# Optimization experiments

Measured on AMD Instinct MI355X. Metric: run time of the kernel, lower is better.

Reference implementation:

```python
import jax, jax.numpy as jnp
import numpy as np

MAX_ITER = 10
EPS = 1e-4


def setup_inputs() -> dict:
    key = jax.random.key(0)
    k1, k2, k3 = jax.random.split(key, 3)
    B, N, M = 64, 1024, 1024
    s = jax.random.uniform(k1, (B, N, M), dtype=jnp.float32)
    nrows = jax.random.randint(k2, (B,), 0, N, dtype=jnp.int64 if jax.config.read('jax_enable_x64') else jnp.int32)
    ncols = jax.random.randint(k3, (B,), 0, M, dtype=nrows.dtype)
    return {"s": s, "nrows": nrows, "ncols": ncols}


def _sinkhorn(s, nrows, ncols):
    # Faithful to torch Sinkhorn.forward with exp=False, dummy_row=False.
    # The torch code builds [B,N,N]/[B,M,M] block-of-ones matrices and matmuls;
    # mathematically this is a masked column-sum (even iters) / row-sum (odd iters)
    # over the valid nrows[b] x ncols[b] block, followed by division inside the
    # block and zeroing outside it.
    B, N, M = s.shape
    row_mask = jnp.arange(N)[None, :] < nrows[:, None]            # [B, N]
    col_mask = jnp.arange(M)[None, :] < ncols[:, None]            # [B, M]
    mask = row_mask[:, :, None] & col_mask[:, None, :]            # [B, N, M]

    out = s + EPS
    for i in range(MAX_ITER):
        if i % 2 == 0:
            # column sums over valid rows -> [B, 1, M]
            sm = jnp.sum(jnp.where(row_mask[:, :, None], out, 0.0), axis=1, keepdims=True)
        else:
            # row sums over valid cols -> [B, N, 1]
            sm = jnp.sum(jnp.where(col_mask[:, None, :], out, 0.0), axis=2, keepdims=True)
        sm = jnp.where(sm == 0, 1.0, sm)  # guard (only affects masked-out entries)
        out = jnp.where(mask, out / sm, 0.0)
    return out


def reference(s, nrows, ncols):
    return _sinkhorn(s, nrows, ncols)
```

## Files before the change

### kernel.cpp

```cpp
#include <hip/hip_runtime.h>
#include <hip/hip_fp16.h>

#define EPS 1e-4f
constexpr int N_DIM  = 1024;
constexpr int M_DIM  = 1024;
constexpr int BATCH  = 64;
constexpr int NB     = 1024;
constexpr int NPHASE = 5;
constexpr int WPAD   = 256;
constexpr int CH     = 16;
constexpr int Q8MIN  = 64;


typedef float v4f __attribute__((ext_vector_type(4)));
__device__ __forceinline__ float4 ntload4(const float* p) {
    v4f v = __builtin_nontemporal_load((const v4f*)p);
    return make_float4(v[0], v[1], v[2], v[3]);
}
__device__ __forceinline__ void ntstore4(float* p, float4 q) {
    v4f v = {q.x, q.y, q.z, q.w};
    __builtin_nontemporal_store(v, (v4f*)p);
}

__device__ __forceinline__ unsigned enc8(float v) {
    int u = (int)__float_as_uint(v) + 0x00040000 - 0x3C000000;
    int b = u >> 19;
    return (unsigned)min(max(b, 16), 127);
}
__device__ __forceinline__ float dec8(unsigned b) {
    return b ? __uint_as_float((b << 19) + 0x3C000000u) : 0.f;
}

__global__ void zero_cnt(unsigned int* cnt) {
    const int t = threadIdx.x;
    if (t < NPHASE * BATCH) cnt[t] = 0u;
}

__device__ __forceinline__ void bat_barrier(unsigned int* cnt, int idx,
                                            unsigned int nact) {
    __syncthreads();
    if (threadIdx.x == 0) {
        __threadfence();
        atomicAdd(&cnt[idx], 1u);
        while (__hip_atomic_load(&cnt[idx], __ATOMIC_ACQUIRE,
                                 __HIP_MEMORY_SCOPE_AGENT) < nact)
            __builtin_amdgcn_s_sleep(8);
    }
    __syncthreads();
    __threadfence();
}

__device__ __forceinline__ void tp_store(__half* tp, size_t idx, float4 v) {
    union { __half2 h2[2]; uint2 u; } pk;
    pk.h2[0] = __floats2half2_rn(v.x, v.y);
    pk.h2[1] = __floats2half2_rn(v.z, v.w);
    *(uint2*)(tp + idx) = pk.u;
}

__global__ __launch_bounds__(256, 4)
void sinkhorn_prop(const float* __restrict__ s,
                   const int* __restrict__ nrows,
                   const int* __restrict__ ncols,
                   __half* __restrict__ h,
                   __half* __restrict__ tp0,
                   __half* __restrict__ tp1,
                   unsigned int* __restrict__ cnt,
                   float* __restrict__ out)
{
    const int tid = threadIdx.x, lane = tid & 63, wv = tid >> 6;
    __shared__ int sR[BATCH];
    __shared__ int sNb[BATCH];
    __shared__ int sPfx[BATCH + 1];

    if (tid < BATCH) sR[tid] = nrows[tid];
    __syncthreads();
    if (tid == 0) {
        long tot = 0;
        for (int i = 0; i < BATCH; ++i) tot += sR[i] + WPAD;
        int acc = 0;
        for (int i = 0; i < BATCH; ++i) {
            int nb = 1 + (int)(((long)(NB - BATCH) * (sR[i] + WPAD)) / tot);
            sNb[i] = nb; sPfx[i] = acc; acc += nb;
        }
        sPfx[BATCH] = acc;
    }
    __syncthreads();

    const int g = blockIdx.x;
    if (g >= sPfx[BATCH]) return;
    int b = BATCH - 1;
    for (int i = 0; i < BATCH; ++i) { if (g < sPfx[i + 1]) { b = i; break; } }
    const int l   = g - sPfx[b];
    const int nbb = sNb[b];
    const int R = sR[b], C = ncols[b];
    const size_t base = (size_t)b * N_DIM * M_DIM;
    const float4 z4 = make_float4(0.f, 0.f, 0.f, 0.f);

    for (int n = R + l; n < N_DIM; n += nbb)
        ntstore4(out + base + (size_t)n * M_DIM + tid * 4, z4);
    if (R == 0) return;

    const int CR = (R + nbb - 1) / nbb;
    const unsigned int nact = (unsigned int)((R + CR - 1) / CR);
    if ((unsigned int)l >= nact) return;
    const int n0 = l * CR;
    const int rows = min(R - n0, CR);
    const bool hi = (C > 512);
    const bool q8 = (R >= Q8MIN && C >= Q8MIN);
    const int g0 = sPfx[b];
    unsigned char* __restrict__ h8 = (unsigned char*)(h + base);

    __shared__ float clds[M_DIM];
    __shared__ float tp_lds[4][M_DIM];

    {
        const int m = tid * 4;
        float4 acc = z4;
        if (m < C) {
            for (int nn = 0; nn < rows; ++nn) {
                const size_t roff = (size_t)(n0 + nn) * M_DIM + m;
                float4 v = ntload4(s + base + roff);
                v.x += EPS;
                v.y = (m + 1 < C) ? v.y + EPS : 0.f;
                v.z = (m + 2 < C) ? v.z + EPS : 0.f;
                v.w = (m + 3 < C) ? v.w + EPS : 0.f;
                acc.x += v.x; acc.y += v.y; acc.z += v.z; acc.w += v.w;
                if (q8) {
                    unsigned b0 = enc8(v.x);
                    unsigned b1 = (v.y > 0.f) ? enc8(v.y) : 0u;
                    unsigned b2 = (v.z > 0.f) ? enc8(v.z) : 0u;
                    unsigned b3 = (v.w > 0.f) ? enc8(v.w) : 0u;
                    *(unsigned*)(h8 + roff) = b0 | (b1 << 8) | (b2 << 16) | (b3 << 24);
                } else {
                    union { __half2 h2[2]; uint2 u2; } pk;
                    pk.h2[0] = __floats2half2_rn(v.x, v.y);
                    pk.h2[1] = __floats2half2_rn(v.z, v.w);
                    *(uint2*)(h + base + roff) = pk.u2;
                }
            }
        } else if (m < 512 || hi) {
            for (int nn = 0; nn < rows; ++nn) {
                const size_t roff = (size_t)(n0 + nn) * M_DIM + m;
                if (q8) *(unsigned*)(h8 + roff) = 0u;
                else    *(uint2*)(h + base + roff) = make_uint2(0u, 0u);
            }
        }
        if (m < 512 || hi)
            tp_store(tp0, (size_t)g * M_DIM + m, acc);
    }
    bat_barrier(cnt, 0 * BATCH + b, nact);

    const __half* tpIn  = tp0;
    __half*       tpOut = tp1;
    float crlo[8], crhi[8];

    for (int step = 0; step < 4; ++step) {
        {
            const int m = tid * 4;
            if (m < 512 || hi) {
                float4 sum = z4;
                for (unsigned int cc = 0; cc < nact; ++cc) {
                    uint2 raw = *(const uint2*)(tpIn + (size_t)(g0 + cc) * M_DIM + m);
                    const __half2* hp = (const __half2*)&raw;
                    float2 f0 = __half22float2(hp[0]);
                    float2 f1 = __half22float2(hp[1]);
                    sum.x += f0.x; sum.y += f0.y; sum.z += f1.x; sum.w += f1.y;
                }
                float4 cv;
                cv.x = (sum.x == 0.f) ? 1.f : 1.f / sum.x;
                cv.y = (sum.y == 0.f) ? 1.f : 1.f / sum.y;
                cv.z = (sum.z == 0.f) ? 1.f : 1.f / sum.z;
                cv.w = (sum.w == 0.f) ? 1.f : 1.f / sum.w;
                *(float4*)&clds[m] = cv;
            }
        }
        __syncthreads();
        {
            float4 a  = *(const float4*)&clds[lane * 8];
            float4 bb = *(const float4*)&clds[lane * 8 + 4];
            crlo[0]=a.x; crlo[1]=a.y; crlo[2]=a.z; crlo[3]=a.w;
            crlo[4]=bb.x; crlo[5]=bb.y; crlo[6]=bb.z; crlo[7]=bb.w;
            if (hi) {
                float4 d = *(const float4*)&clds[512 + lane * 8];
                float4 e = *(const float4*)&clds[512 + lane * 8 + 4];
                crhi[0]=d.x; crhi[1]=d.y; crhi[2]=d.z; crhi[3]=d.w;
                crhi[4]=e.x; crhi[5]=e.y; crhi[6]=e.z; crhi[7]=e.w;
            }
        }

        float tplo[8] = {0,0,0,0,0,0,0,0};
        float tphi[8] = {0,0,0,0,0,0,0,0};

        for (int nn = wv; nn < rows; nn += 4) {
            float flo[8], fhi[8];
            if (q8) {
                const unsigned char* hrow = h8 + (size_t)(n0 + nn) * M_DIM;
                uint2 rlo = *(const uint2*)(hrow + lane * 8);
#pragma unroll
                for (int k = 0; k < 4; ++k) flo[k]     = dec8((rlo.x >> (8*k)) & 0xffu);
#pragma unroll
                for (int k = 0; k < 4; ++k) flo[4 + k] = dec8((rlo.y >> (8*k)) & 0xffu);
                if (hi) {
                    uint2 rhi = *(const uint2*)(hrow + 512 + lane * 8);
#pragma unroll
                    for (int k = 0; k < 4; ++k) fhi[k]     = dec8((rhi.x >> (8*k)) & 0xffu);
#pragma unroll
                    for (int k = 0; k < 4; ++k) fhi[4 + k] = dec8((rhi.y >> (8*k)) & 0xffu);
                }
            } else {
                const __half* hrow = h + base + (size_t)(n0 + nn) * M_DIM;
                uint4 rlo = *(const uint4*)(hrow + lane * 8);
                const __half2* hp = (const __half2*)&rlo;
#pragma unroll
                for (int k = 0; k < 4; ++k) {
                    float2 f = __half22float2(hp[k]);
                    flo[2*k] = f.x; flo[2*k+1] = f.y;
                }
                if (hi) {
                    uint4 rhi = *(const uint4*)(hrow + 512 + lane * 8);
                    const __half2* hq = (const __half2*)&rhi;
#pragma unroll
                    for (int k = 0; k < 4; ++k) {
                        float2 f = __half22float2(hq[k]);
                        fhi[2*k] = f.x; fhi[2*k+1] = f.y;
                    }
                }
            }
            float dot = 0.f;
#pragma unroll
            for (int k = 0; k < 8; ++k) dot += flo[k] * crlo[k];
            if (hi) {
#pragma unroll
                for (int k = 0; k < 8; ++k) dot += fhi[k] * crhi[k];
            }
#pragma unroll
            for (int off = 32; off; off >>= 1) dot += __shfl_xor(dot, off);
            const float r = (dot == 0.f) ? 1.f : 1.f / dot;
#pragma unroll
            for (int k = 0; k < 8; ++k) tplo[k] += flo[k] * r;
            if (hi) {
#pragma unroll
                for (int k = 0; k < 8; ++k) tphi[k] += fhi[k] * r;
            }
        }

#pragma unroll
        for (int k = 0; k < 8; ++k) tp_lds[wv][lane * 8 + k] = tplo[k];
        if (hi) {
#pragma unroll
            for (int k = 0; k < 8; ++k) tp_lds[wv][512 + lane * 8 + k] = tphi[k];
        }
        __syncthreads();
        {
            const int m = tid * 4;
            if (m < 512 || hi) {
                float4 s0 = *(const float4*)&tp_lds[0][m];
                float4 s1 = *(const float4*)&tp_lds[1][m];
                float4 s2 = *(const float4*)&tp_lds[2][m];
                float4 s3 = *(const float4*)&tp_lds[3][m];
                tp_store(tpOut, (size_t)g * M_DIM + m,
                         make_float4(s0.x+s1.x+s2.x+s3.x, s0.y+s1.y+s2.y+s3.y,
                                     s0.z+s1.z+s2.z+s3.z, s0.w+s1.w+s2.w+s3.w));
            }
        }
        bat_barrier(cnt, (1 + step) * BATCH + b, nact);
        const __half* ti = tpOut; tpOut = (__half*)tpIn; tpIn = ti;
    }

    {
        const int m = tid * 4;
        if (m < 512 || hi) {
            float4 sum = z4;
            for (unsigned int cc = 0; cc < nact; ++cc) {
                uint2 raw = *(const uint2*)(tpIn + (size_t)(g0 + cc) * M_DIM + m);
                const __half2* hp = (const __half2*)&raw;
                float2 f0 = __half22float2(hp[0]);
                float2 f1 = __half22float2(hp[1]);
                sum.x += f0.x; sum.y += f0.y; sum.z += f1.x; sum.w += f1.y;
            }
            float4 cv;
            cv.x = (sum.x == 0.f) ? 1.f : 1.f / sum.x;
            cv.y = (sum.y == 0.f) ? 1.f : 1.f / sum.y;
            cv.z = (sum.z == 0.f) ? 1.f : 1.f / sum.z;
            cv.w = (sum.w == 0.f) ? 1.f : 1.f / sum.w;
            *(float4*)&clds[m] = cv;
        }
    }
    __syncthreads();
    {
        float4 a  = *(const float4*)&clds[lane * 8];
        float4 bb = *(const float4*)&clds[lane * 8 + 4];
        crlo[0]=a.x; crlo[1]=a.y; crlo[2]=a.z; crlo[3]=a.w;
        crlo[4]=bb.x; crlo[5]=bb.y; crlo[6]=bb.z; crlo[7]=bb.w;
        if (hi) {
            float4 d = *(const float4*)&clds[512 + lane * 8];
            float4 e = *(const float4*)&clds[512 + lane * 8 + 4];
            crhi[0]=d.x; crhi[1]=d.y; crhi[2]=d.z; crhi[3]=d.w;
            crhi[4]=e.x; crhi[5]=e.y; crhi[6]=e.z; crhi[7]=e.w;
        }
    }
    for (int nn = wv; nn < rows; nn += 4) {
        const int n = n0 + nn;
        float* orow = out + base + (size_t)n * M_DIM;
        float flo[8], fhi[8];
        if (q8) {
            const unsigned char* hrow = h8 + (size_t)n * M_DIM;
            uint2 rlo = *(const uint2*)(hrow + lane * 8);
#pragma unroll
            for (int k = 0; k < 4; ++k) flo[k]     = dec8((rlo.x >> (8*k)) & 0xffu);
#pragma unroll
            for (int k = 0; k < 4; ++k) flo[4 + k] = dec8((rlo.y >> (8*k)) & 0xffu);
            if (hi) {
                uint2 rhi = *(const uint2*)(hrow + 512 + lane * 8);
#pragma unroll
                for (int k = 0; k < 4; ++k) fhi[k]     = dec8((rhi.x >> (8*k)) & 0xffu);
#pragma unroll
                for (int k = 0; k < 4; ++k) fhi[4 + k] = dec8((rhi.y >> (8*k)) & 0xffu);
            }
        } else {
            const __half* hrow = h + base + (size_t)n * M_DIM;
            uint4 rlo = *(const uint4*)(hrow + lane * 8);
            const __half2* hp = (const __half2*)&rlo;
#pragma unroll
            for (int k = 0; k < 4; ++k) {
                float2 f = __half22float2(hp[k]);
                flo[2*k] = f.x; flo[2*k+1] = f.y;
            }
            if (hi) {
                uint4 rhi = *(const uint4*)(hrow + 512 + lane * 8);
                const __half2* hq = (const __half2*)&rhi;
#pragma unroll
                for (int k = 0; k < 4; ++k) {
                    float2 f = __half22float2(hq[k]);
                    fhi[2*k] = f.x; fhi[2*k+1] = f.y;
                }
            }
        }
        float dot = 0.f;
#pragma unroll
        for (int k = 0; k < 8; ++k) dot += flo[k] * crlo[k];
        if (hi) {
#pragma unroll
            for (int k = 0; k < 8; ++k) dot += fhi[k] * crhi[k];
        }
#pragma unroll
        for (int off = 32; off; off >>= 1) dot += __shfl_xor(dot, off);
        const float r = (dot == 0.f) ? 1.f : 1.f / dot;

        ntstore4(orow + lane * 8,     make_float4(flo[0]*r*crlo[0], flo[1]*r*crlo[1],
                                                  flo[2]*r*crlo[2], flo[3]*r*crlo[3]));
        ntstore4(orow + lane * 8 + 4, make_float4(flo[4]*r*crlo[4], flo[5]*r*crlo[5],
                                                  flo[6]*r*crlo[6], flo[7]*r*crlo[7]));
        float4 o2 = z4, o3 = z4;
        if (hi) {
            o2 = make_float4(fhi[0]*r*crhi[0], fhi[1]*r*crhi[1],
                             fhi[2]*r*crhi[2], fhi[3]*r*crhi[3]);
            o3 = make_float4(fhi[4]*r*crhi[4], fhi[5]*r*crhi[5],
                             fhi[6]*r*crhi[6], fhi[7]*r*crhi[7]);
        }
        ntstore4(orow + 512 + lane * 8,     o2);
        ntstore4(orow + 512 + lane * 8 + 4, o3);
    }
}

constexpr int FCROWS = N_DIM / CH;

__global__ __launch_bounds__(256)
void conv_col0(const float* __restrict__ s, const int* __restrict__ nrows,
               const int* __restrict__ ncols, __half* __restrict__ h,
               float* __restrict__ tp0) {
    const int b  = blockIdx.y;
    const int mt = blockIdx.x & 3;
    const int ch = blockIdx.x >> 2;
    const int R = nrows[b], C = ncols[b];
    const int n0 = ch * FCROWS;
    if (n0 >= R) return;
    const int lane = threadIdx.x & 63, wv = threadIdx.x >> 6;
    const int m = mt * 256 + lane * 4;
    const int nend = min(R, n0 + FCROWS);
    const size_t base = (size_t)b * N_DIM * M_DIM;

    float4 acc = make_float4(0.f, 0.f, 0.f, 0.f);
    if (mt * 256 < C) {
        for (int n = n0 + wv; n < nend; n += 4) {
            float4 v = *(const float4*)(s + base + (size_t)n * M_DIM + m);
            v.x = (m + 0 < C) ? v.x + EPS : 0.f;
            v.y = (m + 1 < C) ? v.y + EPS : 0.f;
            v.z = (m + 2 < C) ? v.z + EPS : 0.f;
            v.w = (m + 3 < C) ? v.w + EPS : 0.f;
            acc.x += v.x; acc.y += v.y; acc.z += v.z; acc.w += v.w;
            union { __half2 h2[2]; uint2 u2; } pk;
            pk.h2[0] = __floats2half2_rn(v.x, v.y);
            pk.h2[1] = __floats2half2_rn(v.z, v.w);
            *(uint2*)(h + base + (size_t)n * M_DIM + m) = pk.u2;
        }
    } else {
        const uint2 z = make_uint2(0u, 0u);
        for (int n = n0 + wv; n < nend; n += 4)
            *(uint2*)(h + base + (size_t)n * M_DIM + m) = z;
    }
    __shared__ float4 red[4][64];
    red[wv][lane] = acc;
    __syncthreads();
    if (wv == 0) {
        float4 a0 = red[0][lane], a1 = red[1][lane],
               a2 = red[2][lane], a3 = red[3][lane];
        *(float4*)(tp0 + (size_t)(ch * BATCH + b) * M_DIM + m) =
            make_float4(a0.x+a1.x+a2.x+a3.x, a0.y+a1.y+a2.y+a3.y,
                        a0.z+a1.z+a2.z+a3.z, a0.w+a1.w+a2.w+a3.w);
    }
}

template <bool FINAL>
__global__ __launch_bounds__(256)
void row_step(const __half* __restrict__ h, const int* __restrict__ nrows,
              const int* __restrict__ ncols, const float* __restrict__ tpIn,
              float* __restrict__ tpOut, float* __restrict__ out) {
    const int b  = blockIdx.y;
    const int ch = blockIdx.x;
    const int R = nrows[b], C = ncols[b];
    const int n0 = ch * FCROWS;
    if (!FINAL && n0 >= R) return;
    const int lane = threadIdx.x & 63, wv = threadIdx.x >> 6;
    const size_t base = (size_t)b * N_DIM * M_DIM;
    const bool hi = (C > 512);
    const bool anyrows = (n0 < R);

    __shared__ float clds[M_DIM];
    __shared__ float tp_lds[4][M_DIM];

    float crlo[8], crhi[8];
    if (anyrows) {
        const int nch = min(CH, (R + FCROWS - 1) / FCROWS);
        const int t4 = threadIdx.x * 4;
        if (hi || t4 < 512) {
            float4 sum = make_float4(0.f, 0.f, 0.f, 0.f);
            for (int cc = 0; cc < nch; ++cc) {
                float4 p = *(const float4*)(tpIn + (size_t)(cc * BATCH + b) * M_DIM + t4);
                sum.x += p.x; sum.y += p.y; sum.z += p.z; sum.w += p.w;
            }
            float4 cv;
            cv.x = (sum.x == 0.f) ? 1.f : 1.f / sum.x;
            cv.y = (sum.y == 0.f) ? 1.f : 1.f / sum.y;
            cv.z = (sum.z == 0.f) ? 1.f : 1.f / sum.z;
            cv.w = (sum.w == 0.f) ? 1.f : 1.f / sum.w;
            *(float4*)&clds[t4] = cv;
        }
        __syncthreads();
        float4 a = *(const float4*)&clds[lane * 8];
        float4 bb = *(const float4*)&clds[lane * 8 + 4];
        crlo[0]=a.x; crlo[1]=a.y; crlo[2]=a.z; crlo[3]=a.w;
        crlo[4]=bb.x; crlo[5]=bb.y; crlo[6]=bb.z; crlo[7]=bb.w;
        if (hi) {
            float4 d = *(const float4*)&clds[512 + lane * 8];
            float4 e = *(const float4*)&clds[512 + lane * 8 + 4];
            crhi[0]=d.x; crhi[1]=d.y; crhi[2]=d.z; crhi[3]=d.w;
            crhi[4]=e.x; crhi[5]=e.y; crhi[6]=e.z; crhi[7]=e.w;
        }
    }

    float tplo[8] = {0,0,0,0,0,0,0,0};
    float tphi[8] = {0,0,0,0,0,0,0,0};

    for (int i = 0; i < 16; ++i) {
        const int n = n0 + wv * 16 + i;
        if (n < R) {
            const __half* hrow = h + base + (size_t)n * M_DIM;
            uint4 rlo = *(const uint4*)(hrow + lane * 8);
            float flo[8], fhi[8];
            const __half2* hp = (const __half2*)&rlo;
#pragma unroll
            for (int k = 0; k < 4; ++k) {
                float2 f = __half22float2(hp[k]);
                flo[2*k] = f.x; flo[2*k+1] = f.y;
            }
            float dot = 0.f;
#pragma unroll
            for (int k = 0; k < 8; ++k) dot += flo[k] * crlo[k];
            if (hi) {
                uint4 rhi = *(const uint4*)(hrow + 512 + lane * 8);
                const __half2* hq = (const __half2*)&rhi;
#pragma unroll
                for (int k = 0; k < 4; ++k) {
                    float2 f = __half22float2(hq[k]);
                    fhi[2*k] = f.x; fhi[2*k+1] = f.y;
                }
#pragma unroll
                for (int k = 0; k < 8; ++k) dot += fhi[k] * crhi[k];
            }
#pragma unroll
            for (int off = 32; off; off >>= 1) dot += __shfl_xor(dot, off);
            const float r = (dot == 0.f) ? 1.f : 1.f / dot;

            if (FINAL) {
                float* orow = out + base + (size_t)n * M_DIM;
                *(float4*)(orow + lane * 8)     = make_float4(flo[0]*r*crlo[0], flo[1]*r*crlo[1],
                                                              flo[2]*r*crlo[2], flo[3]*r*crlo[3]);
                *(float4*)(orow + lane * 8 + 4) = make_float4(flo[4]*r*crlo[4], flo[5]*r*crlo[5],
                                                              flo[6]*r*crlo[6], flo[7]*r*crlo[7]);
                float4 o2 = make_float4(0.f,0.f,0.f,0.f), o3 = o2;
                if (hi) {
                    o2 = make_float4(fhi[0]*r*crhi[0], fhi[1]*r*crhi[1],
                                     fhi[2]*r*crhi[2], fhi[3]*r*crhi[3]);
                    o3 = make_float4(fhi[4]*r*crhi[4], fhi[5]*r*crhi[5],
                                     fhi[6]*r*crhi[6], fhi[7]*r*crhi[7]);
                }
                *(float4*)(orow + 512 + lane * 8)     = o2;
                *(float4*)(orow + 512 + lane * 8 + 4) = o3;
            } else {
#pragma unroll
                for (int k = 0; k < 8; ++k) tplo[k] += flo[k] * r;
                if (hi) {
#pragma unroll
                    for (int k = 0; k < 8; ++k) tphi[k] += fhi[k] * r;
                }
            }
        } else if (FINAL) {
            float* orow = out + base + (size_t)n * M_DIM;
            const float4 z = make_float4(0.f, 0.f, 0.f, 0.f);
            *(float4*)(orow + lane * 8)           = z;
            *(float4*)(orow + lane * 8 + 4)       = z;
            *(float4*)(orow + 512 + lane * 8)     = z;
            *(float4*)(orow + 512 + lane * 8 + 4) = z;
        }
    }

    if (!FINAL) {
#pragma unroll
        for (int k = 0; k < 8; ++k) tp_lds[wv][lane * 8 + k] = tplo[k];
        if (hi) {
#pragma unroll
            for (int k = 0; k < 8; ++k) tp_lds[wv][512 + lane * 8 + k] = tphi[k];
        }
        __syncthreads();
        const int t4 = threadIdx.x * 4;
        if (hi || t4 < 512) {
            float4 s0 = *(const float4*)&tp_lds[0][t4];
            float4 s1 = *(const float4*)&tp_lds[1][t4];
            float4 s2 = *(const float4*)&tp_lds[2][t4];
            float4 s3 = *(const float4*)&tp_lds[3][t4];
            *(float4*)(tpOut + (size_t)(ch * BATCH + b) * M_DIM + t4) =
                make_float4(s0.x+s1.x+s2.x+s3.x, s0.y+s1.y+s2.y+s3.y,
                            s0.z+s1.z+s2.z+s3.z, s0.w+s1.w+s2.w+s3.w);
        }
    }
}

extern "C" void kernel_launch(void* const* d_in, const int* in_sizes, int n_in,
                              void* d_out, int out_size, void* d_ws, size_t ws_size,
                              hipStream_t stream) {
    const float* s     = (const float*)d_in[0];
    const int*   nrows = (const int*)d_in[1];
    const int*   ncols = (const int*)d_in[2];
    float*       out   = (float*)d_out;

    const size_t hElems   = (size_t)BATCH * N_DIM * M_DIM;
    const size_t tpRegion = (size_t)16 * 1024 * 1024;
    const size_t need     = hElems * 2 + tpRegion + NPHASE * BATCH * 4;

    if (ws_size >= need) {
        __half* h    = (__half*)d_ws;
        char*   tpRg = (char*)(h + hElems);
        unsigned int* cnt = (unsigned int*)(tpRg + tpRegion);

        int dev = 0, numCU = 0, perCU = 0;
        hipGetDevice(&dev);
        hipDeviceGetAttribute(&numCU, hipDeviceAttributeMultiprocessorCount, dev);
        hipOccupancyMaxActiveBlocksPerMultiprocessor(&perCU, sinkhorn_prop, 256, 0);

        if ((long long)perCU * numCU >= NB) {
            __half* tp0 = (__half*)tpRg;
            __half* tp1 = tp0 + (size_t)NB * M_DIM;
            zero_cnt<<<1, 320, 0, stream>>>(cnt);
            void* args[] = {(void*)&s, (void*)&nrows, (void*)&ncols, (void*)&h,
                            (void*)&tp0, (void*)&tp1, (void*)&cnt, (void*)&out};
            hipLaunchCooperativeKernel((void*)sinkhorn_prop, dim3(NB),
                                       dim3(256), args, 0, stream);
            return;
        }

        float* tp0f = (float*)tpRg;
        float* tp1f = tp0f + (size_t)CH * BATCH * M_DIM;
        dim3 convGrid(4 * CH, BATCH), kGrid(CH, BATCH);
        conv_col0<<<convGrid, 256, 0, stream>>>(s, nrows, ncols, h, tp0f);
        row_step<false><<<kGrid, 256, 0, stream>>>(h, nrows, ncols, tp0f, tp1f, out);
        row_step<false><<<kGrid, 256, 0, stream>>>(h, nrows, ncols, tp1f, tp0f, out);
        row_step<false><<<kGrid, 256, 0, stream>>>(h, nrows, ncols, tp0f, tp1f, out);
        row_step<false><<<kGrid, 256, 0, stream>>>(h, nrows, ncols, tp1f, tp0f, out);
        row_step<true ><<<kGrid, 256, 0, stream>>>(h, nrows, ncols, tp0f, tp1f, out);
        return;
    }
}
```

Measured before the change: 207.5 us.

## Pin each batch's workgroups to one XCD with greedy load-balanced assignment

```diff
diff --git a/kernel.cpp b/kernel.cpp
--- a/kernel.cpp
+++ b/kernel.cpp
@@ -6,6 +6,8 @@
 constexpr int M_DIM  = 1024;
 constexpr int BATCH  = 64;
 constexpr int NB     = 1024;
+constexpr int NXCD   = 8;
+constexpr int SLOTS  = NB / NXCD;
 constexpr int NPHASE = 5;
 constexpr int WPAD   = 256;
 constexpr int CH     = 16;
@@ -58,39 +60,53 @@
 }
 
 __global__ __launch_bounds__(256, 4)
-void sinkhorn_prop(const float* __restrict__ s,
-                   const int* __restrict__ nrows,
-                   const int* __restrict__ ncols,
-                   __half* __restrict__ h,
-                   __half* __restrict__ tp0,
-                   __half* __restrict__ tp1,
-                   unsigned int* __restrict__ cnt,
-                   float* __restrict__ out)
+void sinkhorn_xcd(const float* __restrict__ s,
+                  const int* __restrict__ nrows,
+                  const int* __restrict__ ncols,
+                  __half* __restrict__ h,
+                  __half* __restrict__ tp0,
+                  __half* __restrict__ tp1,
+                  unsigned int* __restrict__ cnt,
+                  float* __restrict__ out)
 {
     const int tid = threadIdx.x, lane = tid & 63, wv = tid >> 6;
     __shared__ int sR[BATCH];
+    __shared__ int sBx[BATCH];
     __shared__ int sNb[BATCH];
-    __shared__ int sPfx[BATCH + 1];
+    __shared__ int sSt[BATCH];
 
     if (tid < BATCH) sR[tid] = nrows[tid];
     __syncthreads();
     if (tid == 0) {
-        long tot = 0;
-        for (int i = 0; i < BATCH; ++i) tot += sR[i] + WPAD;
-        int acc = 0;
+        int load[NXCD]; int W[NXCD]; int Cn[NXCD]; int acc[NXCD];
+        for (int x = 0; x < NXCD; ++x) { load[x] = 0; W[x] = 0; Cn[x] = 0; acc[x] = 0; }
         for (int i = 0; i < BATCH; ++i) {
-            int nb = 1 + (int)(((long)(NB - BATCH) * (sR[i] + WPAD)) / tot);
-            sNb[i] = nb; sPfx[i] = acc; acc += nb;
-        }
-        sPfx[BATCH] = acc;
+            const int w = sR[i] + WPAD;
+            int best = 0;
+            for (int x = 1; x < NXCD; ++x) if (load[x] < load[best]) best = x;
+            sBx[i] = best; load[best] += w;
+        }
+        for (int i = 0; i < BATCH; ++i) { W[sBx[i]] += sR[i] + WPAD; Cn[sBx[i]]++; }
+        for (int i = 0; i < BATCH; ++i) {
+            const int x = sBx[i];
+            int nb = 1 + (int)(((long)(SLOTS - Cn[x]) * (sR[i] + WPAD)) / W[x]);
+            sNb[i] = nb; sSt[i] = acc[x]; acc[x] += nb;
+        }
+        sR[0] = sR[0];
     }
     __syncthreads();
 
-    const int g = blockIdx.x;
-    if (g >= sPfx[BATCH]) return;
-    int b = BATCH - 1;
-    for (int i = 0; i < BATCH; ++i) { if (g < sPfx[i + 1]) { b = i; break; } }
-    const int l   = g - sPfx[b];
+    const int g    = blockIdx.x;
+    const int xcd  = g & (NXCD - 1);
+    const int slot = g >> 3;
+    int b = -1, l = 0;
+    for (int i = 0; i < BATCH; ++i) {
+        if (sBx[i] == xcd && slot >= sSt[i] && slot < sSt[i] + sNb[i]) {
+            b = i; l = slot - sSt[i]; break;
+        }
+    }
+    if (b < 0) return;
+
     const int nbb = sNb[b];
     const int R = sR[b], C = ncols[b];
     const size_t base = (size_t)b * N_DIM * M_DIM;
@@ -107,8 +123,9 @@
     const int rows = min(R - n0, CR);
     const bool hi = (C > 512);
     const bool q8 = (R >= Q8MIN && C >= Q8MIN);
-    const int g0 = sPfx[b];
     unsigned char* __restrict__ h8 = (unsigned char*)(h + base);
+
+    const int tbase0 = xcd * SLOTS + sSt[b];
 
     __shared__ float clds[M_DIM];
     __shared__ float tp_lds[4][M_DIM];
@@ -146,7 +163,7 @@
             }
         }
         if (m < 512 || hi)
-            tp_store(tp0, (size_t)g * M_DIM + m, acc);
+            tp_store(tp0, (size_t)(tbase0 + l) * M_DIM + m, acc);
     }
     bat_barrier(cnt, 0 * BATCH + b, nact);
 
@@ -160,7 +177,7 @@
             if (m < 512 || hi) {
                 float4 sum = z4;
                 for (unsigned int cc = 0; cc < nact; ++cc) {
-                    uint2 raw = *(const uint2*)(tpIn + (size_t)(g0 + cc) * M_DIM + m);
+                    uint2 raw = *(const uint2*)(tpIn + (size_t)(tbase0 + cc) * M_DIM + m);
                     const __half2* hp = (const __half2*)&raw;
                     float2 f0 = __half22float2(hp[0]);
                     float2 f1 = __half22float2(hp[1]);
@@ -258,7 +275,7 @@
                 float4 s1 = *(const float4*)&tp_lds[1][m];
                 float4 s2 = *(const float4*)&tp_lds[2][m];
                 float4 s3 = *(const float4*)&tp_lds[3][m];
-                tp_store(tpOut, (size_t)g * M_DIM + m,
+                tp_store(tpOut, (size_t)(tbase0 + l) * M_DIM + m,
                          make_float4(s0.x+s1.x+s2.x+s3.x, s0.y+s1.y+s2.y+s3.y,
                                      s0.z+s1.z+s2.z+s3.z, s0.w+s1.w+s2.w+s3.w));
             }
@@ -272,7 +289,7 @@
         if (m < 512 || hi) {
             float4 sum = z4;
             for (unsigned int cc = 0; cc < nact; ++cc) {
-                uint2 raw = *(const uint2*)(tpIn + (size_t)(g0 + cc) * M_DIM + m);
+                uint2 raw = *(const uint2*)(tpIn + (size_t)(tbase0 + cc) * M_DIM + m);
                 const __half2* hp = (const __half2*)&raw;
                 float2 f0 = __half22float2(hp[0]);
                 float2 f1 = __half22float2(hp[1]);
@@ -566,7 +583,7 @@
         int dev = 0, numCU = 0, perCU = 0;
         hipGetDevice(&dev);
         hipDeviceGetAttribute(&numCU, hipDeviceAttributeMultiprocessorCount, dev);
-        hipOccupancyMaxActiveBlocksPerMultiprocessor(&perCU, sinkhorn_prop, 256, 0);
+        hipOccupancyMaxActiveBlocksPerMultiprocessor(&perCU, sinkhorn_xcd, 256, 0);
 
         if ((long long)perCU * numCU >= NB) {
             __half* tp0 = (__half*)tpRg;
@@ -574,7 +591,7 @@
             zero_cnt<<<1, 320, 0, stream>>>(cnt);
             void* args[] = {(void*)&s, (void*)&nrows, (void*)&ncols, (void*)&h,
                             (void*)&tp0, (void*)&tp1, (void*)&cnt, (void*)&out};
-            hipLaunchCooperativeKernel((void*)sinkhorn_prop, dim3(NB),
+            hipLaunchCooperativeKernel((void*)sinkhorn_xcd, dim3(NB),
                                        dim3(256), args, 0, stream);
             return;
         }
```

Measured after the change: 204.8 us. No clear change (-1.3%).
